# Optimization experiments

Measured on AMD Instinct MI355X. Metric: run time of the kernel, lower is better.

The kernel has to match this reference:

```python
import jax, jax.numpy as jnp
import numpy as np

DIM = 768
D_STATE = 16
D_INNER = 2 * DIM  # expand=2


def setup_inputs() -> dict:
    key = jax.random.key(0)
    k_x, k_in, k_conv, k_out = jax.random.split(key, 4)
    B, L = 1, 4096
    x = jax.random.normal(k_x, (B, L, DIM), dtype=jnp.float32)
    # torch Linear weight layout: [out_features, in_features]
    W_in = jax.random.normal(k_in, (3 * D_INNER + 2 * D_STATE, DIM), dtype=jnp.float32) * 0.02
    # depthwise conv1d kernel: [out_ch=d_inner, in_ch/groups=1, k=3]
    W_conv = jax.random.normal(k_conv, (D_INNER, 1, 3), dtype=jnp.float32) * 0.1
    W_out = jax.random.normal(k_out, (DIM, D_INNER), dtype=jnp.float32) * 0.02
    A_log = jnp.log(jnp.tile(jnp.arange(1, D_STATE + 1, dtype=jnp.float32), (D_INNER, 1)))
    D = jnp.ones((D_INNER,), dtype=jnp.float32)
    return {"x": x, "W_in": W_in, "W_conv": W_conv, "W_out": W_out, "A_log": A_log, "D": D}


def reference(x, W_in, W_conv, W_out, A_log, D):
    d_inner = W_conv.shape[0]
    d_state = A_log.shape[1]
    Bsz = x.shape[0]

    xz = x @ W_in.T  # [B, L, 3*d_inner + 2*d_state]
    x_inner, z, B_ssm, C_ssm, delta = jnp.split(
        xz, [d_inner, 2 * d_inner, 2 * d_inner + d_state, 2 * d_inner + 2 * d_state], axis=-1
    )

    # depthwise conv over sequence: [B, d_inner, L]
    xc = jax.lax.conv_general_dilated(
        x_inner.transpose(0, 2, 1), W_conv,
        window_strides=(1,), padding=[(1, 1)], feature_group_count=d_inner,
    ).transpose(0, 2, 1)  # back to [B, L, d_inner]
    xc = jax.nn.silu(xc)

    A = -jnp.exp(A_log)  # [d_inner, d_state]
    delta = jax.nn.softplus(delta)  # [B, L, d_inner]
    dA = jnp.exp(jnp.einsum('bld,dn->bldn', delta, A))           # [B, L, d_inner, d_state]
    dBx = jnp.einsum('bld,bln,bld->bldn', delta, B_ssm, xc)      # delta_B * x fused

    def step(h, inp):
        da_t, dbx_t, c_t = inp  # [B,d,n], [B,d,n], [B,n]
        h = da_t * h + dbx_t
        y_t = jnp.einsum('bdn,bn->bd', h, c_t)
        return h, y_t

    h0 = jnp.zeros((Bsz, d_inner, d_state), dtype=x.dtype)
    _, ys = jax.lax.scan(
        step, h0,
        (dA.transpose(1, 0, 2, 3), dBx.transpose(1, 0, 2, 3), C_ssm.transpose(1, 0, 2)),
    )  # ys: [L, B, d_inner]

    y = ys.transpose(1, 0, 2) + xc * D  # skip connection
    y = y * jax.nn.silu(z)
    return y @ W_out.T  # [B, L, dim]
```

## Files before the change

### kernel.cpp

```cpp
#include <hip/hip_runtime.h>
#include <hip/hip_bf16.h>
#include <math.h>

#define LSEQ   4096
#define DIM    768
#define DINNER 1536
#define DSTATE 16
#define NCOLS  4640
#define NCH    256
#define CLEN   16
#define NPAD   4736
#define DXW    1568

typedef _Float16 f16;
typedef __attribute__((ext_vector_type(8))) _Float16 f16x8;
typedef __attribute__((ext_vector_type(4))) float f32x4;

__device__ __forceinline__ void gld_lds16(void* lds_dst, const void* gsrc) {
    __builtin_amdgcn_global_load_lds(
        (__attribute__((address_space(1))) void*)(gsrc),
        (__attribute__((address_space(3))) void*)(lds_dst), 16, 0, 0);
}

#define G1K    768
#define G1_NT  12
#define G1_BM  256
#define G1_BN  128
#define G1_RT  384
#define G1_LDSE (G1_RT * 64)

__global__ __launch_bounds__(512) void gemm1_pipe(const f16* __restrict__ A,
                                                  const f16* __restrict__ B,
                                                  float* __restrict__ C,
                                                  f16* __restrict__ Xb,
                                                  f16* __restrict__ Zb) {
    __shared__ __align__(16) f16 S[3 * G1_LDSE];

    const int P   = gridDim.x >> 3;
    const int idx = (blockIdx.x & 7) * P + (blockIdx.x >> 3);
    const int m0  = (idx & 15) * G1_BM;
    const int n0  = (idx >> 4) * G1_BN;

    const int tid  = threadIdx.x;
    const int w    = tid >> 6;
    const int lane = tid & 63;
    const int wr   = w >> 1;
    const int wc   = w & 1;
    const int m    = lane & 15;
    const int q    = lane >> 4;
    const int rl8  = lane >> 3;
    const int bsel = lane & 7;

    const f16* gb[6];
#pragma unroll
    for (int s = 0; s < 6; ++s) {
        const int rl  = (w + 8 * s) * 8 + rl8;
        const int blk = bsel ^ (rl & 7);
        gb[s] = (rl < G1_BM) ? A + (size_t)(m0 + rl) * G1K + blk * 8
                             : B + (size_t)(n0 + rl - G1_BM) * G1K + blk * 8;
    }

    f32x4 acc[4][4];
#pragma unroll
    for (int i = 0; i < 4; i++)
#pragma unroll
        for (int j = 0; j < 4; j++) acc[i][j] = (f32x4){0.f, 0.f, 0.f, 0.f};

    auto stg2 = [&](int kt, int s0) {
        f16* dst = S + (kt % 3) * G1_LDSE;
#pragma unroll
        for (int s = s0; s < s0 + 2; ++s)
            gld_lds16(dst + (w + 8 * s) * 512, gb[s] + kt * 64);
    };
    auto stg6 = [&](int kt) {
        f16* dst = S + (kt % 3) * G1_LDSE;
#pragma unroll
        for (int s = 0; s < 6; ++s)
            gld_lds16(dst + (w + 8 * s) * 512, gb[s] + kt * 64);
    };

    stg6(0);
    stg6(1);

#pragma unroll
    for (int kt = 0; kt < G1_NT; ++kt) {
        if (kt < G1_NT - 1) asm volatile("s_waitcnt vmcnt(6)" ::: "memory");
        else                asm volatile("s_waitcnt vmcnt(0)" ::: "memory");
        __builtin_amdgcn_s_barrier();
        const f16* As = S + (kt % 3) * G1_LDSE;
        const f16* Bs = As + G1_BM * 64;
        const bool pf = (kt + 2 < G1_NT);

        f16x8 af0[2][2], af2[2][2], bh0[2][2], bh2[2][2];

#pragma unroll
        for (int kk = 0; kk < 2; ++kk) {
            const int fo = (((q + 4 * kk) ^ (m & 7)) << 3);
#pragma unroll
            for (int i = 0; i < 2; ++i) {
                af0[kk][i] = *(const f16x8*)&As[(wr * 64 + i * 16 + m) * 64 + fo];
                bh0[kk][i] = *(const f16x8*)&Bs[(wc * 64 + i * 16 + m) * 64 + fo];
            }
        }
        if (pf) stg2(kt + 2, 0);
        __builtin_amdgcn_s_barrier();
        asm volatile("s_waitcnt lgkmcnt(0)" ::: "memory");
        __builtin_amdgcn_sched_barrier(0);
        __builtin_amdgcn_s_setprio(1);
#pragma unroll
        for (int kk = 0; kk < 2; ++kk)
#pragma unroll
            for (int i = 0; i < 2; ++i)
#pragma unroll
                for (int j = 0; j < 2; ++j)
                    acc[i][j] = __builtin_amdgcn_mfma_f32_16x16x32_f16(
                        af0[kk][i], bh0[kk][j], acc[i][j], 0, 0, 0);
        __builtin_amdgcn_s_setprio(0);

#pragma unroll
        for (int kk = 0; kk < 2; ++kk) {
            const int fo = (((q + 4 * kk) ^ (m & 7)) << 3);
#pragma unroll
            for (int j = 0; j < 2; ++j)
                bh2[kk][j] = *(const f16x8*)&Bs[(wc * 64 + (j + 2) * 16 + m) * 64 + fo];
        }
        if (pf) stg2(kt + 2, 2);
        __builtin_amdgcn_s_barrier();
        asm volatile("s_waitcnt lgkmcnt(0)" ::: "memory");
        __builtin_amdgcn_sched_barrier(0);
        __builtin_amdgcn_s_setprio(1);
#pragma unroll
        for (int kk = 0; kk < 2; ++kk)
#pragma unroll
            for (int i = 0; i < 2; ++i)
#pragma unroll
                for (int j = 0; j < 2; ++j)
                    acc[i][j + 2] = __builtin_amdgcn_mfma_f32_16x16x32_f16(
                        af0[kk][i], bh2[kk][j], acc[i][j + 2], 0, 0, 0);
        __builtin_amdgcn_s_setprio(0);

#pragma unroll
        for (int kk = 0; kk < 2; ++kk) {
            const int fo = (((q + 4 * kk) ^ (m & 7)) << 3);
#pragma unroll
            for (int i = 0; i < 2; ++i)
                af2[kk][i] = *(const f16x8*)&As[(wr * 64 + (i + 2) * 16 + m) * 64 + fo];
        }
        if (pf) stg2(kt + 2, 4);
        __builtin_amdgcn_s_barrier();
        asm volatile("s_waitcnt lgkmcnt(0)" ::: "memory");
        __builtin_amdgcn_sched_barrier(0);
        __builtin_amdgcn_s_setprio(1);
#pragma unroll
        for (int kk = 0; kk < 2; ++kk)
#pragma unroll
            for (int i = 0; i < 2; ++i)
#pragma unroll
                for (int j = 0; j < 2; ++j)
                    acc[i + 2][j] = __builtin_amdgcn_mfma_f32_16x16x32_f16(
                        af2[kk][i], bh0[kk][j], acc[i + 2][j], 0, 0, 0);
        __builtin_amdgcn_s_setprio(0);

        __builtin_amdgcn_s_setprio(1);
#pragma unroll
        for (int kk = 0; kk < 2; ++kk)
#pragma unroll
            for (int i = 0; i < 2; ++i)
#pragma unroll
                for (int j = 0; j < 2; ++j)
                    acc[i + 2][j + 2] = __builtin_amdgcn_mfma_f32_16x16x32_f16(
                        af2[kk][i], bh2[kk][j], acc[i + 2][j + 2], 0, 0, 0);
        __builtin_amdgcn_s_setprio(0);
    }

    if (n0 < DINNER) {
#pragma unroll
        for (int i = 0; i < 4; i++)
#pragma unroll
            for (int j = 0; j < 4; j++) {
                const int col  = n0 + wc * 64 + j * 16 + m;
                const int rowb = m0 + wr * 64 + i * 16 + q * 4;
#pragma unroll
                for (int r = 0; r < 4; r++)
                    Xb[(size_t)(rowb + r) * DINNER + col] = (f16)acc[i][j][r];
            }
        return;
    }
    if (n0 < 2 * DINNER) {
#pragma unroll
        for (int i = 0; i < 4; i++)
#pragma unroll
            for (int j = 0; j < 4; j++) {
                const int col  = n0 - DINNER + wc * 64 + j * 16 + m;
                const int rowb = m0 + wr * 64 + i * 16 + q * 4;
#pragma unroll
                for (int r = 0; r < 4; r++)
                    Zb[(size_t)(rowb + r) * DINNER + col] = (f16)acc[i][j][r];
            }
        return;
    }
#pragma unroll
    for (int i = 0; i < 4; i++)
#pragma unroll
        for (int j = 0; j < 4; j++) {
            const int col = n0 - 2 * DINNER + wc * 64 + j * 16 + m;
            if (col >= DXW) continue;
            const int rowb = m0 + wr * 64 + i * 16 + q * 4;
#pragma unroll
            for (int r = 0; r < 4; r++)
                C[(size_t)(rowb + r) * DXW + col] = acc[i][j][r];
        }
}

template<int BM, int BN, int WM, int WN, int NTB, bool COLM, bool ZMODE>
__global__ __launch_bounds__(256) void gemm_f16(const f16* __restrict__ A,
                                                const f16* __restrict__ B,
                                                float* __restrict__ C,
                                                f16* __restrict__ Xb,
                                                f16* __restrict__ Zb,
                                                int M, int N, int K, int ldc) {
    constexpr int MI  = WM / 16;
    constexpr int NI  = WN / 16;
    constexpr int NWN = BN / WN;
    constexpr int RT  = BM + BN;
    constexpr int NS  = RT / 8;

    __shared__ __align__(16) f16 S[RT * 64];
    f16* As = S;
    f16* Bs = S + BM * 64;

    const int P   = gridDim.x >> 3;
    const int idx = (blockIdx.x & 7) * P + (blockIdx.x >> 3);
    const int m0  = (COLM ? (idx % NTB) : (idx / NTB)) * BM;
    const int n0  = (COLM ? (idx / NTB) : (idx % NTB)) * BN;

    const int tid  = threadIdx.x;
    const int w    = tid >> 6;
    const int lane = tid & 63;
    const int wr   = w / NWN;
    const int wc   = w % NWN;
    const int m    = lane & 15;
    const int q    = lane >> 4;
    const int rl8  = lane >> 3;
    const int bsel = lane & 7;

    f32x4 acc[MI][NI];
#pragma unroll
    for (int i = 0; i < MI; i++)
#pragma unroll
        for (int j = 0; j < NI; j++) acc[i][j] = (f32x4){0.f, 0.f, 0.f, 0.f};

    for (int k0 = 0; k0 < K; k0 += 64) {
#pragma unroll
        for (int t = w; t < NS; t += 4) {
            const int rl  = t * 8 + rl8;
            const int blk = bsel ^ (rl & 7);
            const f16* g = (rl < BM)
                ? A + (size_t)(m0 + rl) * K + k0 + blk * 8
                : B + (size_t)(n0 + rl - BM) * K + k0 + blk * 8;
            gld_lds16(S + t * 8 * 64, g);
        }
        __syncthreads();

#pragma unroll
        for (int kk = 0; kk < 2; kk++) {
            const int fo = (((q + 4 * kk) ^ (m & 7)) << 3);
            f16x8 af[MI], bh[NI];
#pragma unroll
            for (int i = 0; i < MI; i++)
                af[i] = *(const f16x8*)&As[(wr * WM + i * 16 + m) * 64 + fo];
#pragma unroll
            for (int j = 0; j < NI; j++)
                bh[j] = *(const f16x8*)&Bs[(wc * WN + j * 16 + m) * 64 + fo];
#pragma unroll
            for (int i = 0; i < MI; i++)
#pragma unroll
                for (int j = 0; j < NI; j++)
                    acc[i][j] = __builtin_amdgcn_mfma_f32_16x16x32_f16(
                        af[i], bh[j], acc[i][j], 0, 0, 0);
        }
        __syncthreads();
    }

    if (ZMODE && n0 < DINNER) {
#pragma unroll
        for (int i = 0; i < MI; i++)
#pragma unroll
            for (int j = 0; j < NI; j++) {
                const int col  = n0 + wc * WN + j * 16 + m;
                const int rowb = m0 + wr * WM + i * 16 + q * 4;
#pragma unroll
                for (int r = 0; r < 4; r++)
                    Xb[(size_t)(rowb + r) * DINNER + col] = (f16)acc[i][j][r];
            }
        return;
    }
    if (ZMODE && n0 < 2 * DINNER) {
#pragma unroll
        for (int i = 0; i < MI; i++)
#pragma unroll
            for (int j = 0; j < NI; j++) {
                const int col  = n0 - DINNER + wc * WN + j * 16 + m;
                const int rowb = m0 + wr * WM + i * 16 + q * 4;
#pragma unroll
                for (int r = 0; r < 4; r++)
                    Zb[(size_t)(rowb + r) * DINNER + col] = (f16)acc[i][j][r];
            }
        return;
    }
#pragma unroll
    for (int i = 0; i < MI; i++)
#pragma unroll
        for (int j = 0; j < NI; j++) {
            const int col  = (ZMODE ? n0 - 2 * DINNER : n0) + wc * WN + j * 16 + m;
            const int lim  = ZMODE ? DXW : N;
            if (col >= lim) continue;
            const int rowb = m0 + wr * WM + i * 16 + q * 4;
#pragma unroll
            for (int r = 0; r < 4; r++)
                C[(size_t)(rowb + r) * ldc + col] = acc[i][j][r];
        }
}

#define E0 (LSEQ * DIM)
#define E1 (E0 + NPAD * DIM)
#define E2 (E1 + DIM * DINNER)

__global__ __launch_bounds__(256) void cvt_all(const float* __restrict__ x,
                                               const float* __restrict__ Wi,
                                               const float* __restrict__ Wo,
                                               f16* __restrict__ Ax,
                                               f16* __restrict__ Bw,
                                               f16* __restrict__ Bo) {
    int i = (blockIdx.x * 256 + threadIdx.x) * 4;
    if (i < E0) {
        float4 v = *(const float4*)(x + i);
        Ax[i] = (f16)v.x; Ax[i+1] = (f16)v.y; Ax[i+2] = (f16)v.z; Ax[i+3] = (f16)v.w;
    } else if (i < E1) {
        int e = i - E0;
        int n = e / DIM;
        if (n < NCOLS) {
            float4 v = *(const float4*)(Wi + e);
            Bw[e] = (f16)v.x; Bw[e+1] = (f16)v.y; Bw[e+2] = (f16)v.z; Bw[e+3] = (f16)v.w;
        } else {
            Bw[e] = (f16)0.f; Bw[e+1] = (f16)0.f; Bw[e+2] = (f16)0.f; Bw[e+3] = (f16)0.f;
        }
    } else if (i < E2) {
        int e = i - E1;
        float4 v = *(const float4*)(Wo + e);
        Bo[e] = (f16)v.x; Bo[e+1] = (f16)v.y; Bo[e+2] = (f16)v.z; Bo[e+3] = (f16)v.w;
    }
}

__global__ __launch_bounds__(256) void scan1_kernel(const float* __restrict__ Dxz,
                                                    const f16* __restrict__ Xb,
                                                    const float* __restrict__ Wc,
                                                    const float* __restrict__ A_log,
                                                    float* __restrict__ aprod,
                                                    float* __restrict__ hend) {
    __shared__ float Bs[CLEN * DSTATE];
    const int d  = blockIdx.x * 256 + threadIdx.x;
    const int c  = blockIdx.y;
    const int l0 = c * CLEN;
    for (int i = threadIdx.x; i < CLEN * DSTATE; i += 256)
        Bs[i] = Dxz[(size_t)(l0 + (i >> 4)) * DXW + (i & 15)];
    float Areg[DSTATE];
#pragma unroll
    for (int n = 0; n < DSTATE; n++) Areg[n] = -__expf(A_log[d * DSTATE + n]);
    const float w0 = Wc[d * 3 + 0], w1 = Wc[d * 3 + 1], w2 = Wc[d * 3 + 2];
    float xm = (l0 > 0) ? (float)Xb[(size_t)(l0 - 1) * DINNER + d] : 0.f;
    float x0 = (float)Xb[(size_t)l0 * DINNER + d];
    float ld_xp   = (float)Xb[(size_t)(l0 + 1) * DINNER + d];
    float ld_draw = Dxz[(size_t)l0 * DXW + 32 + d];
    __syncthreads();

    float h[DSTATE];
#pragma unroll
    for (int n = 0; n < DSTATE; n++) h[n] = 0.f;
    float S = 0.f;

    for (int t = 0; t < CLEN; t++) {
        const int l = l0 + t;
        float xp = ld_xp, draw = ld_draw;
        if (t + 1 < CLEN) {
            ld_xp   = (l + 2 < LSEQ) ? (float)Xb[(size_t)(l + 2) * DINNER + d] : 0.f;
            ld_draw = Dxz[(size_t)(l + 1) * DXW + 32 + d];
        }
        float v  = xm * w0 + x0 * w1 + xp * w2;
        float xcv = __fdividef(v, 1.f + __expf(-v));
        float dtv = (draw > 20.f) ? draw : __logf(1.f + __expf(draw));
        float u = dtv * xcv;
        S += dtv;
#pragma unroll
        for (int n = 0; n < DSTATE; n++) {
            float e = __expf(dtv * Areg[n]);
            h[n] = e * h[n] + u * Bs[t * DSTATE + n];
        }
        xm = x0; x0 = xp;
    }
#pragma unroll
    for (int n = 0; n < DSTATE; n++) {
        size_t idx = ((size_t)c * DSTATE + n) * DINNER + d;
        aprod[idx] = __expf(S * Areg[n]);
        hend[idx]  = h[n];
    }
}

__global__ __launch_bounds__(256) void scan2_kernel(float* __restrict__ aphi,
                                                    const float* __restrict__ hend) {
    const int g = blockIdx.x * 256 + threadIdx.x;
    const size_t S = (size_t)DSTATE * DINNER;
    float aA[4], eA[4], aB[4], eB[4];
#pragma unroll
    for (int k = 0; k < 4; ++k) {
        aA[k] = aphi[g + (size_t)k * S];
        eA[k] = hend[g + (size_t)k * S];
    }
    float h = 0.f;
    for (int c = 0; c < NCH; c += 8) {
#pragma unroll
        for (int k = 0; k < 4; ++k) {
            aB[k] = aphi[g + (size_t)(c + 4 + k) * S];
            eB[k] = hend[g + (size_t)(c + 4 + k) * S];
        }
#pragma unroll
        for (int k = 0; k < 4; ++k) {
            aphi[g + (size_t)(c + k) * S] = h;
            h = aA[k] * h + eA[k];
        }
        if (c + 8 < NCH) {
#pragma unroll
            for (int k = 0; k < 4; ++k) {
                aA[k] = aphi[g + (size_t)(c + 8 + k) * S];
                eA[k] = hend[g + (size_t)(c + 8 + k) * S];
            }
        }
#pragma unroll
        for (int k = 0; k < 4; ++k) {
            aphi[g + (size_t)(c + 4 + k) * S] = h;
            h = aB[k] * h + eB[k];
        }
    }
}

__global__ __launch_bounds__(256) void scan3_kernel(const float* __restrict__ Dxz,
                                                    const f16* __restrict__ Xb,
                                                    const f16* __restrict__ Zb,
                                                    const float* __restrict__ Wc,
                                                    const float* __restrict__ A_log,
                                                    const float* __restrict__ hinit,
                                                    const float* __restrict__ Dp,
                                                    f16* __restrict__ Ay) {
    __shared__ float Bs[CLEN * DSTATE];
    __shared__ float Cs[CLEN * DSTATE];
    const int d  = blockIdx.x * 256 + threadIdx.x;
    const int c  = blockIdx.y;
    const int l0 = c * CLEN;
    for (int i = threadIdx.x; i < CLEN * DSTATE; i += 256) {
        size_t roff = (size_t)(l0 + (i >> 4)) * DXW;
        Bs[i] = Dxz[roff + (i & 15)];
        Cs[i] = Dxz[roff + 16 + (i & 15)];
    }
    float Areg[DSTATE];
#pragma unroll
    for (int n = 0; n < DSTATE; n++) Areg[n] = -__expf(A_log[d * DSTATE + n]);
    float h[DSTATE];
#pragma unroll
    for (int n = 0; n < DSTATE; n++)
        h[n] = hinit[((size_t)c * DSTATE + n) * DINNER + d];
    const float Dv = Dp[d];
    const float w0 = Wc[d * 3 + 0], w1 = Wc[d * 3 + 1], w2 = Wc[d * 3 + 2];
    float xm = (l0 > 0) ? (float)Xb[(size_t)(l0 - 1) * DINNER + d] : 0.f;
    float x0 = (float)Xb[(size_t)l0 * DINNER + d];
    float ld_xp   = (float)Xb[(size_t)(l0 + 1) * DINNER + d];
    float ld_draw = Dxz[(size_t)l0 * DXW + 32 + d];
    float ld_z    = (float)Zb[(size_t)l0 * DINNER + d];
    __syncthreads();

    for (int t = 0; t < CLEN; t++) {
        const int l = l0 + t;
        float xp = ld_xp, draw = ld_draw, zv = ld_z;
        if (t + 1 < CLEN) {
            ld_xp   = (l + 2 < LSEQ) ? (float)Xb[(size_t)(l + 2) * DINNER + d] : 0.f;
            ld_draw = Dxz[(size_t)(l + 1) * DXW + 32 + d];
            ld_z    = (float)Zb[(size_t)(l + 1) * DINNER + d];
        }
        float v  = xm * w0 + x0 * w1 + xp * w2;
        float xcv = __fdividef(v, 1.f + __expf(-v));
        float dtv = (draw > 20.f) ? draw : __logf(1.f + __expf(draw));
        float u = dtv * xcv;
        float y = 0.f;
#pragma unroll
        for (int n = 0; n < DSTATE; n++) {
            float e = __expf(dtv * Areg[n]);
            h[n] = e * h[n] + u * Bs[t * DSTATE + n];
            y += h[n] * Cs[t * DSTATE + n];
        }
        float sz = __fdividef(zv, 1.f + __expf(-zv));
        Ay[(size_t)l * DINNER + d] = (f16)((y + xcv * Dv) * sz);
        xm = x0; x0 = xp;
    }
}

extern "C" void kernel_launch(void* const* d_in, const int* in_sizes, int n_in,
                              void* d_out, int out_size, void* d_ws, size_t ws_size,
                              hipStream_t stream) {
    const float* x     = (const float*)d_in[0];
    const float* W_in  = (const float*)d_in[1];
    const float* W_conv= (const float*)d_in[2];
    const float* W_out = (const float*)d_in[3];
    const float* A_log = (const float*)d_in[4];
    const float* Dp    = (const float*)d_in[5];
    float* out = (float*)d_out;

    float* ws  = (float*)d_ws;
    float* Dxz = ws;
    float* ap  = Dxz + (size_t)LSEQ * DXW;
    float* he  = ap + (size_t)NCH * DSTATE * DINNER;
    f16* Ax = (f16*)(he + (size_t)NCH * DSTATE * DINNER);
    f16* Ay = Ax + (size_t)LSEQ * DIM;
    f16* Bw = Ay + (size_t)LSEQ * DINNER;
    f16* Bo = Bw + (size_t)NPAD * DIM;
    f16* Zb = Bo + (size_t)DIM * DINNER;
    f16* Xb = Zb + (size_t)LSEQ * DINNER;

    cvt_all<<<E2 / 1024, 256, 0, stream>>>(x, W_in, W_out, Ax, Bw, Bo);

    gemm1_pipe<<<592, 512, 0, stream>>>(Ax, Bw, Dxz, Xb, Zb);

    scan1_kernel<<<dim3(DINNER / 256, NCH), 256, 0, stream>>>(
        Dxz, Xb, W_conv, A_log, ap, he);
    scan2_kernel<<<(DINNER * DSTATE) / 256, 256, 0, stream>>>(ap, he);
    scan3_kernel<<<dim3(DINNER / 256, NCH), 256, 0, stream>>>(
        Dxz, Xb, Zb, W_conv, A_log, ap, Dp, Ay);

    gemm_f16<64, 64, 32, 32, 12, false, false><<<768, 256, 0, stream>>>(
        Ay, Bo, out, nullptr, nullptr, LSEQ, DIM, DINNER, DIM);
}
```

Before: 247.8 us.

## Pipeline output GEMM with triple-buffered async LDS loads and vectorize conversions

Result: faster. 237.6 us (-4.1%).

```diff
diff --git a/kernel.cpp b/kernel.cpp
--- a/kernel.cpp
+++ b/kernel.cpp
@@ -13,6 +13,7 @@
 #define DXW    1568
 
 typedef _Float16 f16;
+typedef __attribute__((ext_vector_type(4))) _Float16 f16x4;
 typedef __attribute__((ext_vector_type(8))) _Float16 f16x8;
 typedef __attribute__((ext_vector_type(4))) float f32x4;
 
@@ -212,113 +213,98 @@
         }
 }
 
-template<int BM, int BN, int WM, int WN, int NTB, bool COLM, bool ZMODE>
-__global__ __launch_bounds__(256) void gemm_f16(const f16* __restrict__ A,
-                                                const f16* __restrict__ B,
-                                                float* __restrict__ C,
-                                                f16* __restrict__ Xb,
-                                                f16* __restrict__ Zb,
-                                                int M, int N, int K, int ldc) {
-    constexpr int MI  = WM / 16;
-    constexpr int NI  = WN / 16;
-    constexpr int NWN = BN / WN;
-    constexpr int RT  = BM + BN;
-    constexpr int NS  = RT / 8;
-
-    __shared__ __align__(16) f16 S[RT * 64];
-    f16* As = S;
-    f16* Bs = S + BM * 64;
+#define G2K    1536
+#define G2_NT  24
+#define G2_LDSE (128 * 64)
+
+__global__ __launch_bounds__(256) void gemm2_pipe(const f16* __restrict__ A,
+                                                  const f16* __restrict__ B,
+                                                  float* __restrict__ C) {
+    __shared__ __align__(16) f16 S[3 * G2_LDSE];
 
     const int P   = gridDim.x >> 3;
     const int idx = (blockIdx.x & 7) * P + (blockIdx.x >> 3);
-    const int m0  = (COLM ? (idx % NTB) : (idx / NTB)) * BM;
-    const int n0  = (COLM ? (idx / NTB) : (idx % NTB)) * BN;
+    const int m0  = (idx / 12) * 64;
+    const int n0  = (idx % 12) * 64;
 
     const int tid  = threadIdx.x;
     const int w    = tid >> 6;
     const int lane = tid & 63;
-    const int wr   = w / NWN;
-    const int wc   = w % NWN;
+    const int wr   = w >> 1;
+    const int wc   = w & 1;
     const int m    = lane & 15;
     const int q    = lane >> 4;
     const int rl8  = lane >> 3;
     const int bsel = lane & 7;
 
-    f32x4 acc[MI][NI];
-#pragma unroll
-    for (int i = 0; i < MI; i++)
-#pragma unroll
-        for (int j = 0; j < NI; j++) acc[i][j] = (f32x4){0.f, 0.f, 0.f, 0.f};
-
-    for (int k0 = 0; k0 < K; k0 += 64) {
-#pragma unroll
-        for (int t = w; t < NS; t += 4) {
-            const int rl  = t * 8 + rl8;
-            const int blk = bsel ^ (rl & 7);
-            const f16* g = (rl < BM)
-                ? A + (size_t)(m0 + rl) * K + k0 + blk * 8
-                : B + (size_t)(n0 + rl - BM) * K + k0 + blk * 8;
-            gld_lds16(S + t * 8 * 64, g);
-        }
-        __syncthreads();
-
-#pragma unroll
-        for (int kk = 0; kk < 2; kk++) {
+    const f16* gb[4];
+#pragma unroll
+    for (int s = 0; s < 4; ++s) {
+        const int rl  = (w + 4 * s) * 8 + rl8;
+        const int blk = bsel ^ (rl & 7);
+        gb[s] = (rl < 64) ? A + (size_t)(m0 + rl) * G2K + blk * 8
+                          : B + (size_t)(n0 + rl - 64) * G2K + blk * 8;
+    }
+
+    f32x4 acc[2][2];
+#pragma unroll
+    for (int i = 0; i < 2; i++)
+#pragma unroll
+        for (int j = 0; j < 2; j++) acc[i][j] = (f32x4){0.f, 0.f, 0.f, 0.f};
+
+    auto stg = [&](int kt) {
+        f16* dst = S + (kt % 3) * G2_LDSE;
+#pragma unroll
+        for (int s = 0; s < 4; ++s)
+            gld_lds16(dst + (w + 4 * s) * 512, gb[s] + kt * 64);
+    };
+
+    stg(0);
+    stg(1);
+
+#pragma unroll
+    for (int kt = 0; kt < G2_NT; ++kt) {
+        if (kt < G2_NT - 1) asm volatile("s_waitcnt vmcnt(4)" ::: "memory");
+        else                asm volatile("s_waitcnt vmcnt(0)" ::: "memory");
+        __builtin_amdgcn_s_barrier();
+        if (kt + 2 < G2_NT) stg(kt + 2);
+
+        const f16* As = S + (kt % 3) * G2_LDSE;
+        const f16* Bs = As + 64 * 64;
+
+        f16x8 af[2][2], bh[2][2];
+#pragma unroll
+        for (int kk = 0; kk < 2; ++kk) {
             const int fo = (((q + 4 * kk) ^ (m & 7)) << 3);
-            f16x8 af[MI], bh[NI];
-#pragma unroll
-            for (int i = 0; i < MI; i++)
-                af[i] = *(const f16x8*)&As[(wr * WM + i * 16 + m) * 64 + fo];
-#pragma unroll
-            for (int j = 0; j < NI; j++)
-                bh[j] = *(const f16x8*)&Bs[(wc * WN + j * 16 + m) * 64 + fo];
-#pragma unroll
-            for (int i = 0; i < MI; i++)
-#pragma unroll
-                for (int j = 0; j < NI; j++)
+#pragma unroll
+            for (int i = 0; i < 2; ++i) {
+                af[kk][i] = *(const f16x8*)&As[(wr * 32 + i * 16 + m) * 64 + fo];
+                bh[kk][i] = *(const f16x8*)&Bs[(wc * 32 + i * 16 + m) * 64 + fo];
+            }
+        }
+        asm volatile("s_waitcnt lgkmcnt(0)" ::: "memory");
+        __builtin_amdgcn_sched_barrier(0);
+        __builtin_amdgcn_s_setprio(1);
+#pragma unroll
+        for (int kk = 0; kk < 2; ++kk)
+#pragma unroll
+            for (int i = 0; i < 2; ++i)
+#pragma unroll
+                for (int j = 0; j < 2; ++j)
                     acc[i][j] = __builtin_amdgcn_mfma_f32_16x16x32_f16(
-                        af[i], bh[j], acc[i][j], 0, 0, 0);
-        }
-        __syncthreads();
-    }
-
-    if (ZMODE && n0 < DINNER) {
-#pragma unroll
-        for (int i = 0; i < MI; i++)
-#pragma unroll
-            for (int j = 0; j < NI; j++) {
-                const int col  = n0 + wc * WN + j * 16 + m;
-                const int rowb = m0 + wr * WM + i * 16 + q * 4;
-#pragma unroll
-                for (int r = 0; r < 4; r++)
-                    Xb[(size_t)(rowb + r) * DINNER + col] = (f16)acc[i][j][r];
-            }
-        return;
-    }
-    if (ZMODE && n0 < 2 * DINNER) {
-#pragma unroll
-        for (int i = 0; i < MI; i++)
-#pragma unroll
-            for (int j = 0; j < NI; j++) {
-                const int col  = n0 - DINNER + wc * WN + j * 16 + m;
-                const int rowb = m0 + wr * WM + i * 16 + q * 4;
-#pragma unroll
-                for (int r = 0; r < 4; r++)
-                    Zb[(size_t)(rowb + r) * DINNER + col] = (f16)acc[i][j][r];
-            }
-        return;
-    }
-#pragma unroll
-    for (int i = 0; i < MI; i++)
-#pragma unroll
-        for (int j = 0; j < NI; j++) {
-            const int col  = (ZMODE ? n0 - 2 * DINNER : n0) + wc * WN + j * 16 + m;
-            const int lim  = ZMODE ? DXW : N;
-            if (col >= lim) continue;
-            const int rowb = m0 + wr * WM + i * 16 + q * 4;
+                        af[kk][i], bh[kk][j], acc[i][j], 0, 0, 0);
+        __builtin_amdgcn_s_setprio(0);
+    }
+
+#pragma unroll
+    for (int i = 0; i < 2; i++)
+#pragma unroll
+        for (int j = 0; j < 2; j++) {
+            const int col  = n0 + wc * 32 + j * 16 + m;
+            const int rowb = m0 + wr * 32 + i * 16 + q * 4;
 #pragma unroll
             for (int r = 0; r < 4; r++)
-                C[(size_t)(rowb + r) * ldc + col] = acc[i][j][r];
+                C[(size_t)(rowb + r) * DIM + col] = acc[i][j][r];
         }
 }
 
@@ -335,20 +321,24 @@
     int i = (blockIdx.x * 256 + threadIdx.x) * 4;
     if (i < E0) {
         float4 v = *(const float4*)(x + i);
-        Ax[i] = (f16)v.x; Ax[i+1] = (f16)v.y; Ax[i+2] = (f16)v.z; Ax[i+3] = (f16)v.w;
+        f16x4 o = {(f16)v.x, (f16)v.y, (f16)v.z, (f16)v.w};
+        *(f16x4*)(Ax + i) = o;
     } else if (i < E1) {
         int e = i - E0;
         int n = e / DIM;
         if (n < NCOLS) {
             float4 v = *(const float4*)(Wi + e);
-            Bw[e] = (f16)v.x; Bw[e+1] = (f16)v.y; Bw[e+2] = (f16)v.z; Bw[e+3] = (f16)v.w;
+            f16x4 o = {(f16)v.x, (f16)v.y, (f16)v.z, (f16)v.w};
+            *(f16x4*)(Bw + e) = o;
         } else {
-            Bw[e] = (f16)0.f; Bw[e+1] = (f16)0.f; Bw[e+2] = (f16)0.f; Bw[e+3] = (f16)0.f;
+            f16x4 o = {(f16)0.f, (f16)0.f, (f16)0.f, (f16)0.f};
+            *(f16x4*)(Bw + e) = o;
         }
     } else if (i < E2) {
         int e = i - E1;
         float4 v = *(const float4*)(Wo + e);
-        Bo[e] = (f16)v.x; Bo[e+1] = (f16)v.y; Bo[e+2] = (f16)v.z; Bo[e+3] = (f16)v.w;
+        f16x4 o = {(f16)v.x, (f16)v.y, (f16)v.z, (f16)v.w};
+        *(f16x4*)(Bo + e) = o;
     }
 }
 
@@ -534,6 +524,5 @@
     scan3_kernel<<<dim3(DINNER / 256, NCH), 256, 0, stream>>>(
         Dxz, Xb, Zb, W_conv, A_log, ap, Dp, Ay);
 
-    gemm_f16<64, 64, 32, 32, 12, false, false><<<768, 256, 0, stream>>>(
-        Ay, Bo, out, nullptr, nullptr, LSEQ, DIM, DINNER, DIM);
-}
+    gemm2_pipe<<<768, 256, 0, stream>>>(Ay, Bo, out);
+}
```
